# Kernel optimization log

Hardware: AMD Instinct MI355X
Metric: run time of the kernel (lower is better)

Reference implementation:

```python
import jax, jax.numpy as jnp
import numpy as np

TOP_K = 8
NUM_EXPERTS = 128
HIDDEN = 2048
TOKENS = 16384
NORM_TOPK_PROB = True


def setup_inputs() -> dict:
    key = jax.random.key(0)
    k1, k2 = jax.random.split(key)
    hidden_states = jax.random.normal(k1, (TOKENS, HIDDEN), dtype=jnp.float32)
    # gate weight [num_experts, hidden] (nn.Linear layout)
    weight = jax.random.normal(k2, (NUM_EXPERTS, HIDDEN), dtype=jnp.float32) * 0.02
    return {"hidden_states": hidden_states, "weight": weight}


def reference(hidden_states, weight):
    x = hidden_states.reshape(-1, HIDDEN)
    # router_logits: [tokens, num_experts]
    router_logits = jnp.einsum("td,ed->te", x, weight)
    router_probs = jax.nn.softmax(router_logits.astype(jnp.float32), axis=-1)
    top_vals, top_idx = jax.lax.top_k(router_probs, TOP_K)
    if NORM_TOPK_PROB:
        top_vals = top_vals / jnp.sum(top_vals, axis=-1, keepdims=True)
    top_vals = top_vals.astype(hidden_states.dtype)
    return router_logits, top_vals, top_idx
```

## Files before the change

kernel.cpp:

```cpp
#include <hip/hip_runtime.h>
#include <float.h>
#include <math.h>

#define TOKENS 16384
#define HIDDEN 2048
#define NEXP 128
#define TOPK 8
#define NCAND 12
#define NSEL 13
#define DELTA 1e-3f

#define BM 32
#define BK 32
#define KITERS (HIDDEN / BK)

typedef float f32x4 __attribute__((ext_vector_type(4)));
typedef short bf16x8 __attribute__((ext_vector_type(8)));

__device__ __forceinline__ unsigned pack_hi(float a, float b) {
    return (__float_as_uint(a) >> 16) | (__float_as_uint(b) & 0xFFFF0000u);
}
__device__ __forceinline__ float resid(float a) {
    return a - __uint_as_float(__float_as_uint(a) & 0xFFFF0000u);
}
__device__ __forceinline__ unsigned short hi16(float a) {
    return (unsigned short)(__float_as_uint(a) >> 16);
}

__device__ __forceinline__ void load_lds_16B(const void* g, void* l) {
    __builtin_amdgcn_global_load_lds(
        (const __attribute__((address_space(1))) unsigned int*)g,
        (__attribute__((address_space(3))) unsigned int*)l, 16, 0, 0);
}

__global__ __launch_bounds__(256) void presplit_w(const float* __restrict__ W,
                                                  unsigned short* __restrict__ Ws) {
    const int c = blockIdx.x * 256 + threadIdx.x;
    const int lane = c & 63;
    const int reg = (c >> 6) & 15;
    const int kt = c >> 10;
    const int nt = reg >> 1, hl = reg & 1;
    const int e = nt * 16 + (lane & 15);
    const int k0 = kt * 32 + (lane >> 4) * 8;
    const float* wp = W + (size_t)e * HIDDEN + k0;
    float4 a = *(const float4*)wp;
    float4 b = *(const float4*)(wp + 4);
    if (hl) {
        a.x = resid(a.x); a.y = resid(a.y); a.z = resid(a.z); a.w = resid(a.w);
        b.x = resid(b.x); b.y = resid(b.y); b.z = resid(b.z); b.w = resid(b.w);
    }
    uint4 o;
    o.x = pack_hi(a.x, a.y); o.y = pack_hi(a.z, a.w);
    o.z = pack_hi(b.x, b.y); o.w = pack_hi(b.z, b.w);
    *(uint4*)(Ws + (size_t)c * 8) = o;
}

__global__ __launch_bounds__(256) void router_gemm(const float* __restrict__ X,
                                                   const unsigned short* __restrict__ Ws,
                                                   float* __restrict__ logits) {
    __shared__ unsigned short sA[2][2 * 2 * 512];
    __shared__ unsigned short sB[2][16 * 512];
    const int tid = threadIdx.x;
    const int lane = tid & 63;
    const int wid = tid >> 6;
    const int wm = wid & 1, wn = wid >> 1;
    const int t0 = blockIdx.x * BM;

    const int arow = tid >> 3, aq = tid & 7;
    const int ag = aq >> 1, ar = arow & 15, am = arow >> 4;
    const int aoff = (ag * 16 + (ar ^ ag)) * 8 + (aq & 1) * 4;
    const int aH = (am * 2 + 0) * 512 + aoff;
    const int aL = (am * 2 + 1) * 512 + aoff;
    const float* Xp = X + (size_t)(t0 + arow) * HIDDEN + aq * 4;

    const int rg = lane >> 4, rr = lane & 15;
    const int aRd = (rg * 16 + (rr ^ rg)) * 8;

    f32x4 acc[4];
#pragma unroll
    for (int nt = 0; nt < 4; ++nt) acc[nt] = (f32x4){0.f, 0.f, 0.f, 0.f};

    {
        const unsigned short* src = Ws + wid * 512 + lane * 8;
        unsigned short* dst = &sB[0][wid * 512];
        load_lds_16B(src, dst);
        load_lds_16B(src + 2048, dst + 2048);
        load_lds_16B(src + 4096, dst + 4096);
        load_lds_16B(src + 6144, dst + 6144);
        const float4 v = *(const float4*)(Xp);
        ushort4 h, l;
        h.x = hi16(v.x); h.y = hi16(v.y); h.z = hi16(v.z); h.w = hi16(v.w);
        l.x = hi16(resid(v.x)); l.y = hi16(resid(v.y));
        l.z = hi16(resid(v.z)); l.w = hi16(resid(v.w));
        *(ushort4*)&sA[0][aH] = h;
        *(ushort4*)&sA[0][aL] = l;
    }
    float4 xv = *(const float4*)(Xp + 32);
    __syncthreads();

#pragma unroll 1
    for (int kt = 0; kt < KITERS; ++kt) {
        const int b = kt & 1;
        if (kt + 1 < KITERS) {
            const unsigned short* src = Ws + (size_t)(kt + 1) * 8192 + wid * 512 + lane * 8;
            unsigned short* dst = &sB[b ^ 1][wid * 512];
            load_lds_16B(src, dst);
            load_lds_16B(src + 2048, dst + 2048);
            load_lds_16B(src + 4096, dst + 4096);
            load_lds_16B(src + 6144, dst + 6144);
            ushort4 h, l;
            h.x = hi16(xv.x); h.y = hi16(xv.y); h.z = hi16(xv.z); h.w = hi16(xv.w);
            l.x = hi16(resid(xv.x)); l.y = hi16(resid(xv.y));
            l.z = hi16(resid(xv.z)); l.w = hi16(resid(xv.w));
            *(ushort4*)&sA[b ^ 1][aH] = h;
            *(ushort4*)&sA[b ^ 1][aL] = l;
        }
        if (kt + 2 < KITERS) xv = *(const float4*)(Xp + (kt + 2) * 32);

        const bf16x8 ah = *(const bf16x8*)&sA[b][(wm * 2 + 0) * 512 + aRd];
        const bf16x8 al = *(const bf16x8*)&sA[b][(wm * 2 + 1) * 512 + aRd];
#pragma unroll
        for (int nt = 0; nt < 4; ++nt) {
            const int rb = ((wn * 4 + nt) * 2) * 512 + lane * 8;
            const bf16x8 bh = *(const bf16x8*)&sB[b][rb];
            const bf16x8 bl = *(const bf16x8*)&sB[b][rb + 512];
            acc[nt] = __builtin_amdgcn_mfma_f32_16x16x32_bf16(ah, bh, acc[nt], 0, 0, 0);
            acc[nt] = __builtin_amdgcn_mfma_f32_16x16x32_bf16(ah, bl, acc[nt], 0, 0, 0);
            acc[nt] = __builtin_amdgcn_mfma_f32_16x16x32_bf16(al, bh, acc[nt], 0, 0, 0);
        }
        __syncthreads();
    }

    const int tr = t0 + wm * 16 + (lane >> 4) * 4;
    const int ec0 = lane & 15;
#pragma unroll
    for (int nt = 0; nt < 4; ++nt) {
        const int e = (wn * 4 + nt) * 16 + ec0;
#pragma unroll
        for (int r = 0; r < 4; ++r)
            logits[(size_t)(tr + r) * NEXP + e] = acc[nt][r];
    }
}

__global__ __launch_bounds__(64) void router_select(const float* __restrict__ logits,
                                                    float* __restrict__ top_vals,
                                                    float* __restrict__ top_idx,
                                                    int* __restrict__ cnt,
                                                    int* __restrict__ list) {
    __shared__ float Ls[64 * 133];
    const int tid = threadIdx.x;
    const int t0 = blockIdx.x * 64;
#pragma unroll
    for (int i = 0; i < 32; ++i) {
        const int idx = i * 64 + tid;
        const int row = idx >> 5, c4 = (idx & 31) * 4;
        const float4 v = *(const float4*)(logits + (size_t)(t0 + row) * NEXP + c4);
        float* d = &Ls[row * 133 + c4];
        d[0] = v.x; d[1] = v.y; d[2] = v.z; d[3] = v.w;
    }
    __syncthreads();

    const float* Lr = &Ls[tid * 133];
    float vals[NSEL]; int idxs[NSEL];
#pragma unroll
    for (int j = 0; j < NSEL; ++j) { vals[j] = -FLT_MAX; idxs[j] = 0; }
    for (int e = 0; e < NEXP; ++e) {
        const float v = Lr[e];
        if (v > vals[NSEL - 1]) {
            int r = 0;
#pragma unroll
            for (int j = 0; j < NSEL; ++j) r += (vals[j] >= v) ? 1 : 0;
#pragma unroll
            for (int j = NSEL - 1; j > 0; --j) {
                const bool c = (j > r);
                vals[j] = c ? vals[j - 1] : vals[j];
                idxs[j] = c ? idxs[j - 1] : idxs[j];
            }
#pragma unroll
            for (int j = 0; j < NSEL; ++j) {
                const bool c = (j == r);
                vals[j] = c ? v : vals[j];
                idxs[j] = c ? e : idxs[j];
            }
        }
    }

    const int t = t0 + tid;
    float ming = FLT_MAX;
#pragma unroll
    for (int i = 0; i < TOPK; ++i) ming = fminf(ming, vals[i] - vals[i + 1]);
    if (ming < DELTA) {
        const int p = atomicAdd(cnt, 1);
        list[p] = t;
    } else {
        const float m = vals[0];
        float ex[TOPK], s = 0.f;
#pragma unroll
        for (int i = 0; i < TOPK; ++i) { ex[i] = expf(vals[i] - m); s += ex[i]; }
        const float inv = 1.f / s;
#pragma unroll
        for (int i = 0; i < TOPK; ++i) {
            top_vals[(size_t)t * TOPK + i] = ex[i] * inv;
            top_idx[(size_t)t * TOPK + i] = (float)idxs[i];
        }
    }
}

__device__ __forceinline__ void top_cand(const float* __restrict__ lrow, int lane,
                                         float* vals, int* idxs) {
    const float l0 = lrow[lane];
    const float l1 = lrow[lane + 64];
    bool r0 = false, r1 = false;
#pragma unroll
    for (int it = 0; it < NCAND; ++it) {
        const float c0 = r0 ? -FLT_MAX : l0;
        const float c1 = r1 ? -FLT_MAX : l1;
        float v; int id;
        if (c1 > c0) { v = c1; id = lane + 64; }
        else         { v = c0; id = lane; }
#pragma unroll
        for (int off = 1; off < 64; off <<= 1) {
            const float ov = __shfl_xor(v, off);
            const int   oi = __shfl_xor(id, off);
            if (ov > v || (ov == v && oi < id)) { v = ov; id = oi; }
        }
        vals[it] = v; idxs[it] = id;
        if (id == lane) r0 = true;
        else if (id == lane + 64) r1 = true;
    }
}

__global__ __launch_bounds__(256) void router_refine(const float* __restrict__ logits,
                                                     const float* __restrict__ X,
                                                     const float* __restrict__ W,
                                                     float* __restrict__ top_vals,
                                                     float* __restrict__ top_idx,
                                                     const int* __restrict__ cnt,
                                                     const int* __restrict__ list) {
    const int lane = threadIdx.x & 63;
    const int gw = blockIdx.x * 4 + (threadIdx.x >> 6);
    const int nwaves = gridDim.x * 4;
    const int n = *cnt;

    for (int ii = gw; ii < n; ii += nwaves) {
        const int t = list[ii];
        float vals[NCAND]; int idxs[NCAND];
        top_cand(logits + (size_t)t * NEXP, lane, vals, idxs);

        const float* xr = X + (size_t)t * HIDDEN;
        double xd[32];
#pragma unroll
        for (int j = 0; j < 8; ++j) {
            const float4 v = *(const float4*)(xr + j * 256 + lane * 4);
            xd[j * 4 + 0] = (double)v.x; xd[j * 4 + 1] = (double)v.y;
            xd[j * 4 + 2] = (double)v.z; xd[j * 4 + 3] = (double)v.w;
        }
        double acc[NCAND];
#pragma unroll
        for (int c = 0; c < NCAND; ++c) {
            const float* wr = W + (size_t)idxs[c] * HIDDEN;
            double a0 = 0.0, a1 = 0.0;
#pragma unroll
            for (int j = 0; j < 8; ++j) {
                const float4 w = *(const float4*)(wr + j * 256 + lane * 4);
                a0 = fma((double)w.x, xd[j * 4 + 0], a0);
                a1 = fma((double)w.y, xd[j * 4 + 1], a1);
                a0 = fma((double)w.z, xd[j * 4 + 2], a0);
                a1 = fma((double)w.w, xd[j * 4 + 3], a1);
            }
            acc[c] = a0 + a1;
        }
#pragma unroll
        for (int c = 0; c < NCAND; ++c)
#pragma unroll
            for (int off = 1; off < 64; off <<= 1)
                acc[c] += __shfl_xor(acc[c], off);

        int rank[NCAND];
#pragma unroll
        for (int c = 0; c < NCAND; ++c) {
            int r = 0;
#pragma unroll
            for (int m = 0; m < NCAND; ++m)
                if (acc[m] > acc[c] || (acc[m] == acc[c] && idxs[m] < idxs[c])) ++r;
            rank[c] = r;
        }
        double vmax = acc[0];
#pragma unroll
        for (int c = 0; c < NCAND; ++c) if (rank[c] == 0) vmax = acc[c];
        float e[NCAND], s = 0.f;
#pragma unroll
        for (int c = 0; c < NCAND; ++c) {
            e[c] = (rank[c] < TOPK) ? expf((float)(acc[c] - vmax)) : 0.f;
            s += e[c];
        }
        const float inv = 1.f / s;
        if (lane == 0) {
#pragma unroll
            for (int c = 0; c < NCAND; ++c)
                if (rank[c] < TOPK) {
                    top_vals[(size_t)t * TOPK + rank[c]] = e[c] * inv;
                    top_idx[(size_t)t * TOPK + rank[c]] = (float)idxs[c];
                }
        }
    }
}

extern "C" void kernel_launch(void* const* d_in, const int* in_sizes, int n_in,
                              void* d_out, int out_size, void* d_ws, size_t ws_size,
                              hipStream_t stream) {
    const float* X = (const float*)d_in[0];
    const float* W = (const float*)d_in[1];
    float* logits = (float*)d_out;
    float* tvals  = logits + (size_t)TOKENS * NEXP;
    float* tidx   = tvals + (size_t)TOKENS * TOPK;

    int* cnt = (int*)d_ws;
    unsigned short* Wsplit = (unsigned short*)((char*)d_ws + 4096);
    int* list = (int*)((char*)d_ws + 4096 + 2 * 1024 * 1024);

    hipMemsetAsync(d_ws, 0, 64, stream);
    presplit_w<<<256, 256, 0, stream>>>(W, Wsplit);
    router_gemm<<<TOKENS / BM, 256, 0, stream>>>(X, Wsplit, logits);
    router_select<<<TOKENS / 64, 64, 0, stream>>>(logits, tvals, tidx, cnt, list);
    router_refine<<<256, 256, 0, stream>>>(logits, X, W, tvals, tidx, cnt, list);
}
```

Baseline: 324.8 us.

## Use 32x32 MFMA with larger tiles and wave-per-token top-k selection

```diff
diff --git a/kernel.cpp b/kernel.cpp
--- a/kernel.cpp
+++ b/kernel.cpp
@@ -7,14 +7,13 @@
 #define NEXP 128
 #define TOPK 8
 #define NCAND 12
-#define NSEL 13
 #define DELTA 1e-3f
 
-#define BM 32
-#define BK 32
+#define BM 64
+#define BK 64
 #define KITERS (HIDDEN / BK)
 
-typedef float f32x4 __attribute__((ext_vector_type(4)));
+typedef float f32x16 __attribute__((ext_vector_type(16)));
 typedef short bf16x8 __attribute__((ext_vector_type(8)));
 
 __device__ __forceinline__ unsigned pack_hi(float a, float b) {
@@ -22,9 +21,6 @@
 }
 __device__ __forceinline__ float resid(float a) {
     return a - __uint_as_float(__float_as_uint(a) & 0xFFFF0000u);
-}
-__device__ __forceinline__ unsigned short hi16(float a) {
-    return (unsigned short)(__float_as_uint(a) >> 16);
 }
 
 __device__ __forceinline__ void load_lds_16B(const void* g, void* l) {
@@ -37,11 +33,12 @@
                                                   unsigned short* __restrict__ Ws) {
     const int c = blockIdx.x * 256 + threadIdx.x;
     const int lane = c & 63;
-    const int reg = (c >> 6) & 15;
-    const int kt = c >> 10;
-    const int nt = reg >> 1, hl = reg & 1;
-    const int e = nt * 16 + (lane & 15);
-    const int k0 = kt * 32 + (lane >> 4) * 8;
+    const int q = c >> 6;
+    const int hl = q & 1;
+    const int nt = (q >> 1) & 3;
+    const int k16 = q >> 3;
+    const int e = nt * 32 + (lane & 31);
+    const int k0 = k16 * 16 + (lane >> 5) * 8;
     const float* wp = W + (size_t)e * HIDDEN + k0;
     float4 a = *(const float4*)wp;
     float4 b = *(const float4*)(wp + 4);
@@ -58,141 +55,132 @@
 __global__ __launch_bounds__(256) void router_gemm(const float* __restrict__ X,
                                                    const unsigned short* __restrict__ Ws,
                                                    float* __restrict__ logits) {
-    __shared__ unsigned short sA[2][2 * 2 * 512];
-    __shared__ unsigned short sB[2][16 * 512];
+    __shared__ unsigned short sA[16 * 512];
+    __shared__ unsigned short sB[32 * 512];
     const int tid = threadIdx.x;
     const int lane = tid & 63;
     const int wid = tid >> 6;
     const int wm = wid & 1, wn = wid >> 1;
     const int t0 = blockIdx.x * BM;
 
-    const int arow = tid >> 3, aq = tid & 7;
-    const int ag = aq >> 1, ar = arow & 15, am = arow >> 4;
-    const int aoff = (ag * 16 + (ar ^ ag)) * 8 + (aq & 1) * 4;
-    const int aH = (am * 2 + 0) * 512 + aoff;
-    const int aL = (am * 2 + 1) * 512 + aoff;
-    const float* Xp = X + (size_t)(t0 + arow) * HIDDEN + aq * 4;
-
-    const int rg = lane >> 4, rr = lane & 15;
-    const int aRd = (rg * 16 + (rr ^ rg)) * 8;
-
-    f32x4 acc[4];
-#pragma unroll
-    for (int nt = 0; nt < 4; ++nt) acc[nt] = (f32x4){0.f, 0.f, 0.f, 0.f};
-
-    {
-        const unsigned short* src = Ws + wid * 512 + lane * 8;
-        unsigned short* dst = &sB[0][wid * 512];
-        load_lds_16B(src, dst);
-        load_lds_16B(src + 2048, dst + 2048);
-        load_lds_16B(src + 4096, dst + 4096);
-        load_lds_16B(src + 6144, dst + 6144);
-        const float4 v = *(const float4*)(Xp);
-        ushort4 h, l;
-        h.x = hi16(v.x); h.y = hi16(v.y); h.z = hi16(v.z); h.w = hi16(v.w);
-        l.x = hi16(resid(v.x)); l.y = hi16(resid(v.y));
-        l.z = hi16(resid(v.z)); l.w = hi16(resid(v.w));
-        *(ushort4*)&sA[0][aH] = h;
-        *(ushort4*)&sA[0][aL] = l;
-    }
-    float4 xv = *(const float4*)(Xp + 32);
-    __syncthreads();
+    const int swm = tid >> 7, ss = (tid >> 5) & 3, stok = tid & 31;
+    const float* Xp = X + (size_t)(t0 + swm * 32 + stok) * HIDDEN + ss * 16;
+    const int cA0 = ((swm * 4 + ss) * 2) * 512;
+
+    f32x16 acc[2];
+#pragma unroll
+    for (int i = 0; i < 2; ++i)
+#pragma unroll
+        for (int r = 0; r < 16; ++r) acc[i][r] = 0.f;
+
+    float4 xv0 = *(const float4*)(Xp);
+    float4 xv1 = *(const float4*)(Xp + 4);
+    float4 xv2 = *(const float4*)(Xp + 8);
+    float4 xv3 = *(const float4*)(Xp + 12);
 
 #pragma unroll 1
     for (int kt = 0; kt < KITERS; ++kt) {
-        const int b = kt & 1;
+        __syncthreads();
+        {
+            const unsigned short* src = Ws + ((size_t)kt * 32 + wid * 8) * 512 + lane * 8;
+            unsigned short* dst = &sB[(wid * 8) * 512];
+#pragma unroll
+            for (int i = 0; i < 8; ++i)
+                load_lds_16B(src + i * 512, dst + i * 512);
+        }
+        {
+            uint4 v;
+            v.x = pack_hi(xv0.x, xv0.y); v.y = pack_hi(xv0.z, xv0.w);
+            v.z = pack_hi(xv1.x, xv1.y); v.w = pack_hi(xv1.z, xv1.w);
+            *(uint4*)&sA[cA0 + stok * 8] = v;
+            v.x = pack_hi(xv2.x, xv2.y); v.y = pack_hi(xv2.z, xv2.w);
+            v.z = pack_hi(xv3.x, xv3.y); v.w = pack_hi(xv3.z, xv3.w);
+            *(uint4*)&sA[cA0 + (32 + stok) * 8] = v;
+            v.x = pack_hi(resid(xv0.x), resid(xv0.y)); v.y = pack_hi(resid(xv0.z), resid(xv0.w));
+            v.z = pack_hi(resid(xv1.x), resid(xv1.y)); v.w = pack_hi(resid(xv1.z), resid(xv1.w));
+            *(uint4*)&sA[cA0 + 512 + stok * 8] = v;
+            v.x = pack_hi(resid(xv2.x), resid(xv2.y)); v.y = pack_hi(resid(xv2.z), resid(xv2.w));
+            v.z = pack_hi(resid(xv3.x), resid(xv3.y)); v.w = pack_hi(resid(xv3.z), resid(xv3.w));
+            *(uint4*)&sA[cA0 + 512 + (32 + stok) * 8] = v;
+        }
+        __syncthreads();
+
         if (kt + 1 < KITERS) {
-            const unsigned short* src = Ws + (size_t)(kt + 1) * 8192 + wid * 512 + lane * 8;
-            unsigned short* dst = &sB[b ^ 1][wid * 512];
-            load_lds_16B(src, dst);
-            load_lds_16B(src + 2048, dst + 2048);
-            load_lds_16B(src + 4096, dst + 4096);
-            load_lds_16B(src + 6144, dst + 6144);
-            ushort4 h, l;
-            h.x = hi16(xv.x); h.y = hi16(xv.y); h.z = hi16(xv.z); h.w = hi16(xv.w);
-            l.x = hi16(resid(xv.x)); l.y = hi16(resid(xv.y));
-            l.z = hi16(resid(xv.z)); l.w = hi16(resid(xv.w));
-            *(ushort4*)&sA[b ^ 1][aH] = h;
-            *(ushort4*)&sA[b ^ 1][aL] = l;
-        }
-        if (kt + 2 < KITERS) xv = *(const float4*)(Xp + (kt + 2) * 32);
-
-        const bf16x8 ah = *(const bf16x8*)&sA[b][(wm * 2 + 0) * 512 + aRd];
-        const bf16x8 al = *(const bf16x8*)&sA[b][(wm * 2 + 1) * 512 + aRd];
-#pragma unroll
-        for (int nt = 0; nt < 4; ++nt) {
-            const int rb = ((wn * 4 + nt) * 2) * 512 + lane * 8;
-            const bf16x8 bh = *(const bf16x8*)&sB[b][rb];
-            const bf16x8 bl = *(const bf16x8*)&sB[b][rb + 512];
-            acc[nt] = __builtin_amdgcn_mfma_f32_16x16x32_bf16(ah, bh, acc[nt], 0, 0, 0);
-            acc[nt] = __builtin_amdgcn_mfma_f32_16x16x32_bf16(ah, bl, acc[nt], 0, 0, 0);
-            acc[nt] = __builtin_amdgcn_mfma_f32_16x16x32_bf16(al, bh, acc[nt], 0, 0, 0);
-        }
-        __syncthreads();
-    }
-
-    const int tr = t0 + wm * 16 + (lane >> 4) * 4;
-    const int ec0 = lane & 15;
-#pragma unroll
-    for (int nt = 0; nt < 4; ++nt) {
-        const int e = (wn * 4 + nt) * 16 + ec0;
-#pragma unroll
-        for (int r = 0; r < 4; ++r)
-            logits[(size_t)(tr + r) * NEXP + e] = acc[nt][r];
-    }
-}
-
-__global__ __launch_bounds__(64) void router_select(const float* __restrict__ logits,
-                                                    float* __restrict__ top_vals,
-                                                    float* __restrict__ top_idx,
-                                                    int* __restrict__ cnt,
-                                                    int* __restrict__ list) {
-    __shared__ float Ls[64 * 133];
-    const int tid = threadIdx.x;
-    const int t0 = blockIdx.x * 64;
-#pragma unroll
-    for (int i = 0; i < 32; ++i) {
-        const int idx = i * 64 + tid;
-        const int row = idx >> 5, c4 = (idx & 31) * 4;
-        const float4 v = *(const float4*)(logits + (size_t)(t0 + row) * NEXP + c4);
-        float* d = &Ls[row * 133 + c4];
-        d[0] = v.x; d[1] = v.y; d[2] = v.z; d[3] = v.w;
-    }
-    __syncthreads();
-
-    const float* Lr = &Ls[tid * 133];
-    float vals[NSEL]; int idxs[NSEL];
-#pragma unroll
-    for (int j = 0; j < NSEL; ++j) { vals[j] = -FLT_MAX; idxs[j] = 0; }
-    for (int e = 0; e < NEXP; ++e) {
-        const float v = Lr[e];
-        if (v > vals[NSEL - 1]) {
-            int r = 0;
-#pragma unroll
-            for (int j = 0; j < NSEL; ++j) r += (vals[j] >= v) ? 1 : 0;
-#pragma unroll
-            for (int j = NSEL - 1; j > 0; --j) {
-                const bool c = (j > r);
-                vals[j] = c ? vals[j - 1] : vals[j];
-                idxs[j] = c ? idxs[j - 1] : idxs[j];
+            const float* xp = Xp + (kt + 1) * BK;
+            xv0 = *(const float4*)(xp);
+            xv1 = *(const float4*)(xp + 4);
+            xv2 = *(const float4*)(xp + 8);
+            xv3 = *(const float4*)(xp + 12);
+        }
+
+#pragma unroll
+        for (int s = 0; s < 4; ++s) {
+            const int ab = ((wm * 4 + s) * 2) * 512 + lane * 8;
+            const bf16x8 ah = *(const bf16x8*)&sA[ab];
+            const bf16x8 al = *(const bf16x8*)&sA[ab + 512];
+#pragma unroll
+            for (int ntl = 0; ntl < 2; ++ntl) {
+                const int nt = wn * 2 + ntl;
+                const int bb = ((s * 4 + nt) * 2) * 512 + lane * 8;
+                const bf16x8 bh = *(const bf16x8*)&sB[bb];
+                const bf16x8 bl = *(const bf16x8*)&sB[bb + 512];
+                acc[ntl] = __builtin_amdgcn_mfma_f32_32x32x16_bf16(ah, bh, acc[ntl], 0, 0, 0);
+                acc[ntl] = __builtin_amdgcn_mfma_f32_32x32x16_bf16(ah, bl, acc[ntl], 0, 0, 0);
+                acc[ntl] = __builtin_amdgcn_mfma_f32_32x32x16_bf16(al, bh, acc[ntl], 0, 0, 0);
             }
-#pragma unroll
-            for (int j = 0; j < NSEL; ++j) {
-                const bool c = (j == r);
-                vals[j] = c ? v : vals[j];
-                idxs[j] = c ? e : idxs[j];
-            }
-        }
-    }
-
-    const int t = t0 + tid;
+        }
+    }
+
+    const int col = lane & 31;
+    const int rbase = 4 * (lane >> 5);
+#pragma unroll
+    for (int ntl = 0; ntl < 2; ++ntl) {
+        const int e = wn * 64 + ntl * 32 + col;
+#pragma unroll
+        for (int reg = 0; reg < 16; ++reg) {
+            const int row = (reg & 3) + 8 * (reg >> 2) + rbase;
+            logits[(size_t)(t0 + wm * 32 + row) * NEXP + e] = acc[ntl][reg];
+        }
+    }
+}
+
+__global__ __launch_bounds__(256) void router_select(const float* __restrict__ logits,
+                                                     float* __restrict__ top_vals,
+                                                     float* __restrict__ top_idx,
+                                                     int* __restrict__ cnt,
+                                                     int* __restrict__ list) {
+    const int lane = threadIdx.x & 63;
+    const int t = blockIdx.x * 4 + (threadIdx.x >> 6);
+    const float* lrow = logits + (size_t)t * NEXP;
+    const float l0 = lrow[lane];
+    const float l1 = lrow[lane + 64];
+    bool r0 = false, r1 = false;
+    float vals[TOPK + 1]; int idxs[TOPK + 1];
+#pragma unroll
+    for (int it = 0; it < TOPK + 1; ++it) {
+        const float c0 = r0 ? -FLT_MAX : l0;
+        const float c1 = r1 ? -FLT_MAX : l1;
+        float v; int id;
+        if (c1 > c0) { v = c1; id = lane + 64; }
+        else         { v = c0; id = lane; }
+#pragma unroll
+        for (int off = 1; off < 64; off <<= 1) {
+            const float ov = __shfl_xor(v, off);
+            const int   oi = __shfl_xor(id, off);
+            if (ov > v || (ov == v && oi < id)) { v = ov; id = oi; }
+        }
+        vals[it] = v; idxs[it] = id;
+        if (id == lane) r0 = true;
+        else if (id == lane + 64) r1 = true;
+    }
+
     float ming = FLT_MAX;
 #pragma unroll
     for (int i = 0; i < TOPK; ++i) ming = fminf(ming, vals[i] - vals[i + 1]);
+
     if (ming < DELTA) {
-        const int p = atomicAdd(cnt, 1);
-        list[p] = t;
-    } else {
+        if (lane == 0) { const int p = atomicAdd(cnt, 1); list[p] = t; }
+    } else if (lane == 0) {
         const float m = vals[0];
         float ex[TOPK], s = 0.f;
 #pragma unroll
@@ -322,6 +310,6 @@
     hipMemsetAsync(d_ws, 0, 64, stream);
     presplit_w<<<256, 256, 0, stream>>>(W, Wsplit);
     router_gemm<<<TOKENS / BM, 256, 0, stream>>>(X, Wsplit, logits);
-    router_select<<<TOKENS / 64, 64, 0, stream>>>(logits, tvals, tidx, cnt, list);
+    router_select<<<TOKENS / 4, 256, 0, stream>>>(logits, tvals, tidx, cnt, list);
     router_refine<<<256, 256, 0, stream>>>(logits, X, W, tvals, tidx, cnt, list);
 }
```

New measurement: 326.4 us. Within noise of the previous version (+0.5%).
